# Kernel tuning notes

Measured on AMD Instinct MI355X. Metric: run time of the kernel, lower is better.

## Reference

```python
import jax, jax.numpy as jnp
import numpy as np

N_NODES = 50000
N_EDGES = 600000
D = 128
LN_EPS = 1e-5


def setup_inputs() -> dict:
    key = jax.random.key(0)
    ks = jax.random.split(key, 10)
    s = 1.0 / np.sqrt(D)
    return {
        "node_reps": jax.random.normal(ks[0], (N_NODES, D), jnp.float32),
        "edge_reps": jax.random.normal(ks[1], (N_EDGES, D), jnp.float32),
        "src_idx": jax.random.randint(ks[2], (N_EDGES,), 0, N_NODES, jnp.int32),
        "dst_idx": jnp.sort(jax.random.randint(ks[3], (N_EDGES,), 0, N_NODES, jnp.int32)),
        "Wq": jax.random.normal(ks[4], (D, D), jnp.float32) * s,
        "Wk": jax.random.normal(ks[5], (D, D), jnp.float32) * s,
        "Wv": jax.random.normal(ks[6], (D, D), jnp.float32) * s,
        "Wo": jax.random.normal(ks[7], (D, D), jnp.float32) * s,
        "ln_gamma": jnp.ones((D,), jnp.float32),
        "ln_beta": jnp.zeros((D,), jnp.float32),
        "W1": jax.random.normal(ks[8], (3 * D, D), jnp.float32) * (1.0 / np.sqrt(3 * D)),
        "b1": jnp.zeros((D,), jnp.float32),
        "W2": jax.random.normal(ks[9], (D, D), jnp.float32) * s,
        "b2": jnp.zeros((D,), jnp.float32),
    }


def _layer_norm(x, g, b):
    mu = jnp.mean(x, axis=-1, keepdims=True)
    var = jnp.mean(jnp.square(x - mu), axis=-1, keepdims=True)
    return (x - mu) * jax.lax.rsqrt(var + LN_EPS) * g + b


def reference(node_reps, edge_reps, src_idx, dst_idx, Wq, Wk, Wv, Wo,
              ln_gamma, ln_beta, W1, b1, W2, b2):
    n_nodes, d = node_reps.shape
    # dense projections once per node (kernel-friendly GEMMs)
    q = node_reps @ Wq                                  # [N, d]
    k_nodes = node_reps @ Wk                            # [N, d]
    v_nodes = node_reps @ Wv                            # [N, d]
    # per-edge gather + edge bias
    k_e = k_nodes[src_idx] + edge_reps                  # [E, d]
    scores = jnp.sum(q[dst_idx] * k_e, axis=-1) / jnp.sqrt(jnp.float32(d))  # [E]
    # segment softmax over edges sharing the same dst node
    seg_max = jax.ops.segment_max(scores, dst_idx, num_segments=n_nodes)
    ex = jnp.exp(scores - seg_max[dst_idx])
    denom = jax.ops.segment_sum(ex, dst_idx, num_segments=n_nodes)
    alpha = ex / denom[dst_idx]                          # [E]
    v_e = v_nodes[src_idx] + edge_reps                   # [E, d]
    agg = jax.ops.segment_sum(alpha[:, None] * v_e, dst_idx, num_segments=n_nodes)  # [N, d]
    updated = _layer_norm(node_reps + agg @ Wo, ln_gamma, ln_beta)  # [N, d]
    # triplet fusion MLP over (dst node, edge, src node)
    h_trip = jnp.concatenate([node_reps[dst_idx], edge_reps, node_reps[src_idx]], axis=-1)  # [E, 3d]
    fused = jax.nn.relu(h_trip @ W1 + b1) @ W2 + b2      # [E, d]
    return updated, fused
```

## Files before the change

### kernel.cpp

```cpp
#include <hip/hip_runtime.h>
#include <hip/hip_bf16.h>

#define NN 50000
#define NE 600000
#define D 128

typedef __bf16 bf16x8 __attribute__((ext_vector_type(8)));
typedef __bf16 bf16x4 __attribute__((ext_vector_type(4)));
typedef float f32x4 __attribute__((ext_vector_type(4)));

#define MFMA(a, b, c) __builtin_amdgcn_mfma_f32_16x16x32_bf16((a), (b), (c), 0, 0, 0)


static __device__ __forceinline__ bf16x8 load_a_frag_nc(const float* __restrict__ A,
                                                        int row, int k0) {
  const f32x4* p = (const f32x4*)(A + (size_t)row * D + k0);
  f32x4 v0 = p[0], v1 = p[1];
  bf16x8 r;
  r[0] = (__bf16)v0[0]; r[1] = (__bf16)v0[1]; r[2] = (__bf16)v0[2]; r[3] = (__bf16)v0[3];
  r[4] = (__bf16)v1[0]; r[5] = (__bf16)v1[1]; r[6] = (__bf16)v1[2]; r[7] = (__bf16)v1[3];
  return r;
}

static __device__ __forceinline__ void stage_a_tile128(const float* __restrict__ A, int M,
                                                       int row_base, char* lds, int tid) {
  const int l32 = tid & 31;
  const int g = tid >> 5;
#pragma unroll
  for (int it = 0; it < 16; ++it) {
    int rl = it * 8 + g;
    int r = row_base + rl;
    f32x4 v = {};
    if (r < M) v = *(const f32x4*)(A + (size_t)r * D + l32 * 4);
    bf16x4 b;
    b[0] = (__bf16)v[0]; b[1] = (__bf16)v[1]; b[2] = (__bf16)v[2]; b[3] = (__bf16)v[3];
    int byte = (rl * 256 + l32 * 8) ^ ((rl & 7) << 4);
    *(bf16x4*)(lds + byte) = b;
  }
}

static __device__ __forceinline__ bf16x8 read_a_frag(const char* lds, int rl, int k0) {
  int byte = (rl * 256 + k0 * 2) ^ ((rl & 7) << 4);
  return *(const bf16x8*)(lds + byte);
}

template <int CTRL>
static __device__ __forceinline__ float dpp_add(float x) {
  int v = __builtin_amdgcn_update_dpp(0, __float_as_int(x), CTRL, 0xf, 0xf, true);
  return x + __int_as_float(v);
}

static __device__ __forceinline__ float red32(float x) {
  x = dpp_add<0xB1>(x);
  x = dpp_add<0x4E>(x);
  x = dpp_add<0x124>(x);
  x = dpp_add<0x128>(x);
  return x + __shfl_xor(x, 16, 64);
}

#define CATT 0.12751744612764933f

struct PrepArgs {
  const float* W[8];
  __bf16* WT[8];
  const int* dst;
  int* offs;
};

__global__ void prep_all(PrepArgs pa) {
  int b = blockIdx.x;
  if (b < 512) {
    int w = b >> 6;
    int t = (b & 63) * 256 + threadIdx.x;
    int n = t & 127, k = t >> 7;
    float v = pa.W[w][k * 128 + n];
    if (w == 0) v *= CATT;
    pa.WT[w][n * 128 + k] = (__bf16)v;
  } else {
    int n = (b - 512) * 256 + threadIdx.x;
    if (n > NN) return;
    int lo = 0, hi = NE;
    while (lo < hi) {
      int mid = (lo + hi) >> 1;
      if (pa.dst[mid] < n) lo = mid + 1; else hi = mid;
    }
    pa.offs[n] = lo;
  }
}

struct GemmBatch {
  const __bf16* BT[5];
  void* C[5];
  const float* bias[5];
  int mode[5];
};

__global__ __launch_bounds__(256) void gemm_k128_b(const float* __restrict__ A,
                                                   GemmBatch gb, int M) {
  __shared__ __align__(16) char atile[128 * 256];
  const int y = blockIdx.y;
  const __bf16* __restrict__ BT = gb.BT[y];
  const int tid = threadIdx.x;
  const int lane = tid & 63;
  const int wave = tid >> 6;
  const int wr = wave >> 1, wc = wave & 1;
  const int row0 = blockIdx.x * 128;
  const int col0 = wc * 64;
  const int lr = lane & 15;
  const int lk = (lane >> 4) << 3;

  stage_a_tile128(A, M, row0, atile, tid);
  __syncthreads();

  f32x4 acc[4][4] = {};
#pragma unroll
  for (int kk = 0; kk < 4; ++kk) {
    const int k0 = kk * 32 + lk;
    bf16x8 a[4], b[4];
#pragma unroll
    for (int m = 0; m < 4; ++m) a[m] = read_a_frag(atile, wr * 64 + m * 16 + lr, k0);
#pragma unroll
    for (int n = 0; n < 4; ++n) b[n] = *(const bf16x8*)(BT + (size_t)(col0 + n * 16 + lr) * D + k0);
#pragma unroll
    for (int m = 0; m < 4; ++m)
#pragma unroll
      for (int n = 0; n < 4; ++n)
        acc[m][n] = MFMA(a[m], b[n], acc[m][n]);
  }
  const int rr = (lane >> 4) * 4;
  float bv[4] = {0.f, 0.f, 0.f, 0.f};
  if (gb.bias[y]) {
#pragma unroll
    for (int n = 0; n < 4; ++n) bv[n] = gb.bias[y][col0 + n * 16 + lr];
  }
  const int mode = gb.mode[y];
#pragma unroll
  for (int m = 0; m < 4; ++m)
#pragma unroll
    for (int j = 0; j < 4; ++j) {
      const int row = row0 + wr * 64 + m * 16 + rr + j;
      if (row < M) {
#pragma unroll
        for (int n = 0; n < 4; ++n) {
          const int c = col0 + n * 16 + lr;
          const float val = acc[m][n][j] + bv[n];
          if (mode == 0) {
            ((float*)gb.C[y])[(size_t)row * D + c] = val;
          } else if (mode == 1) {
            ((__bf16*)gb.C[y])[(size_t)row * D + c] = (__bf16)val;
          } else {
            const int e = ((c >> 2) << 3) + (c & 3) + (mode == 3 ? 4 : 0);
            ((__bf16*)gb.C[y])[(size_t)row * 256 + e] = (__bf16)val;
          }
        }
      }
    }
}

__global__ __launch_bounds__(256) void edge_mlp(
    const float* __restrict__ edge,
    const __bf16* __restrict__ W1bT,
    const __bf16* __restrict__ W2T,
    const __bf16* __restrict__ P1,
    const __bf16* __restrict__ P3,
    const int* __restrict__ dst,
    const int* __restrict__ src,
    const float* __restrict__ b2,
    float* __restrict__ out_fused) {
  __shared__ __align__(16) char buf[64 * 256];
  const int tid = threadIdx.x;
  const int eb = blockIdx.x * 64;
  const int lane = tid & 63;
  const int wave = tid >> 6;
  const int wr = wave >> 1, wc = wave & 1;
  const int lr = lane & 15;
  const int lk = (lane >> 4) << 3;
  const int col0 = wc * 64;
  const int rr = (lane >> 4) * 4;

  f32x4 acc[2][4] = {};
#pragma unroll
  for (int kk = 0; kk < 4; ++kk) {
    const int k0 = kk * 32 + lk;
    bf16x8 a[2], bm[4];
#pragma unroll
    for (int m = 0; m < 2; ++m) a[m] = load_a_frag_nc(edge, eb + wr * 32 + m * 16 + lr, k0);
#pragma unroll
    for (int n = 0; n < 4; ++n) bm[n] = *(const bf16x8*)(W1bT + (size_t)(col0 + n * 16 + lr) * D + k0);
#pragma unroll
    for (int m = 0; m < 2; ++m)
#pragma unroll
      for (int n = 0; n < 4; ++n)
        acc[m][n] = MFMA(a[m], bm[n], acc[m][n]);
  }

#pragma unroll
  for (int m = 0; m < 2; ++m) {
#pragma unroll
    for (int j = 0; j < 4; ++j) {
      const int rl = wr * 32 + m * 16 + rr + j;
      const __bf16* __restrict__ p1r = P1 + (size_t)dst[eb + rl] * D;
      const __bf16* __restrict__ p3r = P3 + (size_t)src[eb + rl] * D;
#pragma unroll
      for (int n = 0; n < 4; ++n) {
        const int c = col0 + n * 16 + lr;
        float v = fmaxf(acc[m][n][j] + (float)p1r[c] + (float)p3r[c], 0.f);
        int byte = (rl * 256 + c * 2) ^ ((rl & 7) << 4);
        *(__bf16*)(buf + byte) = (__bf16)v;
      }
    }
  }
  __syncthreads();

  float b2v[4];
#pragma unroll
  for (int n = 0; n < 4; ++n) b2v[n] = b2[col0 + n * 16 + lr];
  f32x4 acc2[2][4] = {};
#pragma unroll
  for (int kk = 0; kk < 4; ++kk) {
    const int k0 = kk * 32 + lk;
    bf16x8 a[2], bm[4];
#pragma unroll
    for (int m = 0; m < 2; ++m) a[m] = read_a_frag(buf, wr * 32 + m * 16 + lr, k0);
#pragma unroll
    for (int n = 0; n < 4; ++n) bm[n] = *(const bf16x8*)(W2T + (size_t)(col0 + n * 16 + lr) * D + k0);
#pragma unroll
    for (int m = 0; m < 2; ++m)
#pragma unroll
      for (int n = 0; n < 4; ++n)
        acc2[m][n] = MFMA(a[m], bm[n], acc2[m][n]);
  }
#pragma unroll
  for (int m = 0; m < 2; ++m)
#pragma unroll
    for (int j = 0; j < 4; ++j) {
      int rl = wr * 32 + m * 16 + rr + j;
      int e = eb + rl;
#pragma unroll
      for (int n = 0; n < 4; ++n) {
        int c = col0 + n * 16 + lr;
        out_fused[(size_t)e * D + c] = acc2[m][n][j] + b2v[n];
      }
    }
}

#define LD1(P, K, J, SV)                                                     \
  do {                                                                       \
    const int jj_ = (J);                                                     \
    const int jc_ = jj_ < jm ? jj_ : 0;                                      \
    int si_ = __shfl((SV), jj_ & 31, 32);                                    \
    si_ = jj_ < jm ? si_ : 0;                                                \
    kv##P[K] = *(const bf16x8*)(KV + (size_t)si_ * 256 + (l32 << 3));        \
    ee##P[K] = *(const f32x4*)(edge + (size_t)(s0 + jc_) * D + (l32 << 2));  \
  } while (0)

#define LOADC(P, C)                                                          \
  do {                                                                       \
    const int c4_ = (C) * 4;                                                 \
    const int sv_ = (c4_ < 32) ? sidx0 : sidx1;                              \
    LD1(P, 0, c4_ + 0, sv_); LD1(P, 1, c4_ + 1, sv_);                        \
    LD1(P, 2, c4_ + 2, sv_); LD1(P, 3, c4_ + 3, sv_);                        \
  } while (0)

#define CP1(P, K, J)                                                         \
  do {                                                                       \
    const int jj_ = (J);                                                     \
    f32x4 ef_ = ee##P[K];                                                    \
    float x0_ = (float)kv##P[K][0] + ef_[0];                                 \
    float x1_ = (float)kv##P[K][1] + ef_[1];                                 \
    float x2_ = (float)kv##P[K][2] + ef_[2];                                 \
    float x3_ = (float)kv##P[K][3] + ef_[3];                                 \
    float pp_ = fmaf(qs[1], x1_, qs[0] * x0_) + fmaf(qs[3], x3_, qs[2] * x2_); \
    float s_ = red32(pp_);                                                   \
    float w_ = jj_ < jm ? exp2f(s_) : 0.f;                                   \
    l += w_;                                                                 \
    a[0] = fmaf(w_, (float)kv##P[K][4] + ef_[0], a[0]);                      \
    a[1] = fmaf(w_, (float)kv##P[K][5] + ef_[1], a[1]);                      \
    a[2] = fmaf(w_, (float)kv##P[K][6] + ef_[2], a[2]);                      \
    a[3] = fmaf(w_, (float)kv##P[K][7] + ef_[3], a[3]);                      \
  } while (0)

#define COMPC(P, C)                                                          \
  do {                                                                       \
    const int cc4_ = (C) * 4;                                                \
    CP1(P, 0, cc4_ + 0); CP1(P, 1, cc4_ + 1);                                \
    CP1(P, 2, cc4_ + 2); CP1(P, 3, cc4_ + 3);                                \
  } while (0)

__global__ __launch_bounds__(256) __attribute__((amdgpu_waves_per_eu(3)))
void attn_node(
    const float* __restrict__ edge,
    const int* __restrict__ src,
    const float* __restrict__ Q,
    const __bf16* __restrict__ KV,
    const int* __restrict__ offs,
    const __bf16* __restrict__ WoT,
    const float* __restrict__ noderep,
    const float* __restrict__ gamma,
    const float* __restrict__ beta,
    float* __restrict__ out_updated) {
  __shared__ __align__(16) char buf[8192];
  const int tid = threadIdx.x;
  const int nw = tid >> 5;
  const int node = blockIdx.x * 8 + nw;
  const int l32 = tid & 31;
  int s0 = offs[node], s1 = offs[node + 1];
  int cnt = s1 - s0;
  f32x4 qs = *(const f32x4*)(Q + (size_t)node * D + l32 * 4);
  float l = 0.f;
  f32x4 a = {0.f, 0.f, 0.f, 0.f};

  const int jm = cnt < 64 ? cnt : 64;
  if (jm > 0) {
    int sidx0 = 0, sidx1 = 0;
    if (l32 < cnt) sidx0 = src[s0 + l32];
    if (l32 + 32 < cnt) sidx1 = src[s0 + 32 + l32];
    bf16x8 kv0[4], kv1[4];
    f32x4 ee0[4], ee1[4];
    const int nch = (jm + 3) >> 2;
    LOADC(0, 0);
    for (int c = 0; c < nch; c += 2) {
      if (c + 1 < nch) LOADC(1, c + 1);
      COMPC(0, c);
      if (c + 2 < nch) LOADC(0, c + 2);
      if (c + 1 < nch) COMPC(1, c + 1);
    }
    for (int i = 64; i < cnt; ++i) {
      int si = src[s0 + i];
      bf16x8 kvx = *(const bf16x8*)(KV + (size_t)si * 256 + (l32 << 3));
      f32x4 ef = *(const f32x4*)(edge + (size_t)(s0 + i) * D + (l32 << 2));
      float x0 = (float)kvx[0] + ef[0], x1 = (float)kvx[1] + ef[1];
      float x2 = (float)kvx[2] + ef[2], x3 = (float)kvx[3] + ef[3];
      float pp = fmaf(qs[1], x1, qs[0] * x0) + fmaf(qs[3], x3, qs[2] * x2);
      float w = exp2f(red32(pp));
      l += w;
      a[0] = fmaf(w, (float)kvx[4] + ef[0], a[0]);
      a[1] = fmaf(w, (float)kvx[5] + ef[1], a[1]);
      a[2] = fmaf(w, (float)kvx[6] + ef[2], a[2]);
      a[3] = fmaf(w, (float)kvx[7] + ef[3], a[3]);
    }
  }
  float inv = l > 0.f ? 1.f / l : 0.f;
  f32x4 r;
  r[0] = a[0] * inv; r[1] = a[1] * inv; r[2] = a[2] * inv; r[3] = a[3] * inv;

  {
    bf16x4 rb;
    rb[0] = (__bf16)r[0]; rb[1] = (__bf16)r[1];
    rb[2] = (__bf16)r[2]; rb[3] = (__bf16)r[3];
    int byte = (nw * 256 + l32 * 8) ^ ((nw & 7) << 4);
    *(bf16x4*)(buf + byte) = rb;
  }
  __syncthreads();

  {
    const int wave = tid >> 6;
    const int lane = tid & 63;
    const int lr = lane & 15;
    const int lk = (lane >> 4) << 3;
    f32x4 acc[2] = {};
#pragma unroll
    for (int kk = 0; kk < 4; ++kk) {
      int k0 = kk * 32 + lk;
      bf16x8 af = read_a_frag(buf, lr, k0);
#pragma unroll
      for (int tt = 0; tt < 2; ++tt) {
        int nn = wave * 2 + tt;
        bf16x8 bm = *(const bf16x8*)(WoT + (size_t)(nn * 16 + lr) * D + k0);
        acc[tt] = MFMA(af, bm, acc[tt]);
      }
    }
    float* xl = (float*)(buf + 4096);
    const int rr = (lane >> 4) * 4;
    if (rr < 8) {
#pragma unroll
      for (int tt = 0; tt < 2; ++tt) {
        int nn = wave * 2 + tt;
#pragma unroll
        for (int j = 0; j < 4; ++j)
          xl[(rr + j) * 128 + nn * 16 + lr] = acc[tt][j];
      }
    }
  }
  __syncthreads();

  {
    const float* xl = (const float*)(buf + 4096);
    f32x4 xv = *(const f32x4*)(xl + nw * 128 + l32 * 4);
    f32x4 nv = *(const f32x4*)(noderep + (size_t)node * D + l32 * 4);
    float x0 = xv[0] + nv[0], x1 = xv[1] + nv[1];
    float x2 = xv[2] + nv[2], x3 = xv[3] + nv[3];
    float s = red32(x0 + x1 + x2 + x3);
    float mu = s * (1.f / 128.f);
    float d0 = x0 - mu, d1 = x1 - mu, d2 = x2 - mu, d3 = x3 - mu;
    float vv = red32(d0 * d0 + d1 * d1 + d2 * d2 + d3 * d3);
    float rstd = rsqrtf(vv * (1.f / 128.f) + 1e-5f);
    f32x4 g = *(const f32x4*)(gamma + l32 * 4);
    f32x4 bb = *(const f32x4*)(beta + l32 * 4);
    f32x4 o;
    o[0] = d0 * rstd * g[0] + bb[0];
    o[1] = d1 * rstd * g[1] + bb[1];
    o[2] = d2 * rstd * g[2] + bb[2];
    o[3] = d3 * rstd * g[3] + bb[3];
    *(f32x4*)(out_updated + (size_t)node * D + l32 * 4) = o;
  }
}

extern "C" void kernel_launch(void* const* d_in, const int* in_sizes, int n_in,
                              void* d_out, int out_size, void* d_ws, size_t ws_size,
                              hipStream_t stream) {
  const float* node = (const float*)d_in[0];
  const float* edge = (const float*)d_in[1];
  const int* src = (const int*)d_in[2];
  const int* dst = (const int*)d_in[3];
  const float* Wq = (const float*)d_in[4];
  const float* Wk = (const float*)d_in[5];
  const float* Wv = (const float*)d_in[6];
  const float* Wo = (const float*)d_in[7];
  const float* gamma = (const float*)d_in[8];
  const float* beta = (const float*)d_in[9];
  const float* W1 = (const float*)d_in[10];
  const float* b1 = (const float*)d_in[11];
  const float* W2 = (const float*)d_in[12];
  const float* b2 = (const float*)d_in[13];

  float* out_updated = (float*)d_out;
  float* out_fused = (float*)d_out + (size_t)NN * D;

  char* ws = (char*)d_ws;
  size_t o = 0;
  auto take = [&](size_t bytes) {
    char* p = ws + o;
    o = (o + bytes + 255) & ~(size_t)255;
    return p;
  };
  int* offs = (int*)take((NN + 1) * sizeof(int));
  __bf16* WqT = (__bf16*)take(128 * 128 * 2);
  __bf16* WkT = (__bf16*)take(128 * 128 * 2);
  __bf16* WvT = (__bf16*)take(128 * 128 * 2);
  __bf16* WoT = (__bf16*)take(128 * 128 * 2);
  __bf16* W1aT = (__bf16*)take(128 * 128 * 2);
  __bf16* W1bT = (__bf16*)take(128 * 128 * 2);
  __bf16* W1cT = (__bf16*)take(128 * 128 * 2);
  __bf16* W2T = (__bf16*)take(128 * 128 * 2);
  float* Qb = (float*)take((size_t)NN * D * 4);
  __bf16* KVb = (__bf16*)take((size_t)NN * 256 * 2);
  __bf16* P1b = (__bf16*)take((size_t)NN * D * 2);
  __bf16* P3b = (__bf16*)take((size_t)NN * D * 2);

  PrepArgs pa;
  pa.W[0] = Wq; pa.WT[0] = WqT;
  pa.W[1] = Wk; pa.WT[1] = WkT;
  pa.W[2] = Wv; pa.WT[2] = WvT;
  pa.W[3] = Wo; pa.WT[3] = WoT;
  pa.W[4] = W1; pa.WT[4] = W1aT;
  pa.W[5] = W1 + 128 * 128; pa.WT[5] = W1bT;
  pa.W[6] = W1 + 256 * 128; pa.WT[6] = W1cT;
  pa.W[7] = W2; pa.WT[7] = W2T;
  pa.dst = dst; pa.offs = offs;
  prep_all<<<512 + (NN + 256) / 256, 256, 0, stream>>>(pa);

  int gnode = (NN + 127) / 128;
  GemmBatch gb;
  gb.BT[0] = WqT;  gb.C[0] = Qb;  gb.bias[0] = nullptr; gb.mode[0] = 0;
  gb.BT[1] = WkT;  gb.C[1] = KVb; gb.bias[1] = nullptr; gb.mode[1] = 2;
  gb.BT[2] = WvT;  gb.C[2] = KVb; gb.bias[2] = nullptr; gb.mode[2] = 3;
  gb.BT[3] = W1aT; gb.C[3] = P1b; gb.bias[3] = b1;      gb.mode[3] = 1;
  gb.BT[4] = W1cT; gb.C[4] = P3b; gb.bias[4] = nullptr; gb.mode[4] = 1;
  gemm_k128_b<<<dim3(gnode, 5), 256, 0, stream>>>(node, gb, NN);

  edge_mlp<<<NE / 64, 256, 0, stream>>>(edge, W1bT, W2T, P1b, P3b, dst, src,
                                        b2, out_fused);
  attn_node<<<NN / 8, 256, 0, stream>>>(edge, src, Qb, KVb, offs,
                                        WoT, node, gamma, beta, out_updated);
}
```

Before: 471.1 us.

## Prefetch gathered P1/P3 rows into LDS via async global_load_lds in edge_mlp

Before the first GEMM, the edge MLP kernel now issues asynchronous global-to-LDS loads of the gathered P1[dst] and P3[src] rows into two LDS buffers, so these gathers overlap with the first MFMA loop. The old path did scalar bf16 gathers from global memory in the epilogue. It also remaps block indices with an XCD-style swizzle (8 groups of 1172) and pads the grid to 9376 blocks, with early exit for out-of-range blocks. The cost is double the LDS per block and an extra barrier, which may reduce occupancy.

Result: no change. 462.4 us (-1.8%).

```diff
diff --git a/kernel.cpp b/kernel.cpp
--- a/kernel.cpp
+++ b/kernel.cpp
@@ -11,6 +11,12 @@
 
 #define MFMA(a, b, c) __builtin_amdgcn_mfma_f32_16x16x32_bf16((a), (b), (c), 0, 0, 0)
 
+
+static __device__ __forceinline__ void gload_lds16(const void* g, void* l) {
+  __builtin_amdgcn_global_load_lds(
+      (const __attribute__((address_space(1))) unsigned int*)g,
+      (__attribute__((address_space(3))) unsigned int*)l, 16, 0, 0);
+}
 
 static __device__ __forceinline__ bf16x8 load_a_frag_nc(const float* __restrict__ A,
                                                         int row, int k0) {
@@ -167,9 +173,12 @@
     const int* __restrict__ src,
     const float* __restrict__ b2,
     float* __restrict__ out_fused) {
-  __shared__ __align__(16) char buf[64 * 256];
+  __shared__ __align__(16) char bufA[64 * 256];
+  __shared__ __align__(16) char bufB[64 * 256];
   const int tid = threadIdx.x;
-  const int eb = blockIdx.x * 64;
+  const int swz = (blockIdx.x & 7) * 1172 + (blockIdx.x >> 3);
+  if (swz >= NE / 64) return;
+  const int eb = swz * 64;
   const int lane = tid & 63;
   const int wave = tid >> 6;
   const int wr = wave >> 1, wc = wave & 1;
@@ -178,6 +187,27 @@
   const int col0 = wc * 64;
   const int rr = (lane >> 4) * 4;
 
+  {
+    const int gr = lane >> 4;
+    const int slot = lane & 15;
+    int di[4], sg[4];
+#pragma unroll
+    for (int c = 0; c < 4; ++c) {
+      int rl = wave * 16 + c * 4 + gr;
+      di[c] = dst[eb + rl];
+      sg[c] = src[eb + rl];
+    }
+#pragma unroll
+    for (int c = 0; c < 4; ++c) {
+      int rl = wave * 16 + c * 4 + gr;
+      int sb = (slot * 16) ^ ((rl & 7) << 4);
+      gload_lds16((const char*)(P1 + (size_t)di[c] * D) + sb,
+                  bufA + (wave * 16 + c * 4) * 256);
+      gload_lds16((const char*)(P3 + (size_t)sg[c] * D) + sb,
+                  bufB + (wave * 16 + c * 4) * 256);
+    }
+  }
+
   f32x4 acc[2][4] = {};
 #pragma unroll
   for (int kk = 0; kk < 4; ++kk) {
@@ -193,20 +223,21 @@
       for (int n = 0; n < 4; ++n)
         acc[m][n] = MFMA(a[m], bm[n], acc[m][n]);
   }
+  __syncthreads();
 
 #pragma unroll
   for (int m = 0; m < 2; ++m) {
 #pragma unroll
     for (int j = 0; j < 4; ++j) {
       const int rl = wr * 32 + m * 16 + rr + j;
-      const __bf16* __restrict__ p1r = P1 + (size_t)dst[eb + rl] * D;
-      const __bf16* __restrict__ p3r = P3 + (size_t)src[eb + rl] * D;
 #pragma unroll
       for (int n = 0; n < 4; ++n) {
         const int c = col0 + n * 16 + lr;
-        float v = fmaxf(acc[m][n][j] + (float)p1r[c] + (float)p3r[c], 0.f);
         int byte = (rl * 256 + c * 2) ^ ((rl & 7) << 4);
-        *(__bf16*)(buf + byte) = (__bf16)v;
+        float g1 = (float)*(const __bf16*)(bufA + byte);
+        float g3 = (float)*(const __bf16*)(bufB + byte);
+        float v = fmaxf(acc[m][n][j] + g1 + g3, 0.f);
+        *(__bf16*)(bufA + byte) = (__bf16)v;
       }
     }
   }
@@ -221,7 +252,7 @@
     const int k0 = kk * 32 + lk;
     bf16x8 a[2], bm[4];
 #pragma unroll
-    for (int m = 0; m < 2; ++m) a[m] = read_a_frag(buf, wr * 32 + m * 16 + lr, k0);
+    for (int m = 0; m < 2; ++m) a[m] = read_a_frag(bufA, wr * 32 + m * 16 + lr, k0);
 #pragma unroll
     for (int n = 0; n < 4; ++n) bm[n] = *(const bf16x8*)(W2T + (size_t)(col0 + n * 16 + lr) * D + k0);
 #pragma unroll
@@ -469,8 +500,8 @@
   gb.BT[4] = W1cT; gb.C[4] = P3b; gb.bias[4] = nullptr; gb.mode[4] = 1;
   gemm_k128_b<<<dim3(gnode, 5), 256, 0, stream>>>(node, gb, NN);
 
-  edge_mlp<<<NE / 64, 256, 0, stream>>>(edge, W1bT, W2T, P1b, P3b, dst, src,
-                                        b2, out_fused);
+  edge_mlp<<<9376, 256, 0, stream>>>(edge, W1bT, W2T, P1b, P3b, dst, src,
+                                     b2, out_fused);
   attn_node<<<NN / 8, 256, 0, stream>>>(edge, src, Qb, KVb, offs,
                                         WoT, node, gamma, beta, out_updated);
 }
```
